# Performance work log

Hardware: AMD Instinct MI355X
Metric: run time of the kernel (lower is better)

The kernel has to match this reference:

```python
import jax, jax.numpy as jnp
import numpy as np

N, E, D, L = 20000, 320000, 3072, 64
H = D // 2  # 1536
EPS = 1e-5


def setup_inputs() -> dict:
    key = jax.random.key(0)
    ks = jax.random.split(key, 16)
    inp = {
        "x": jax.random.normal(ks[0], (N, D), dtype=jnp.float32),
        "edge_index": jax.random.randint(ks[1], (2, E), 0, N, dtype=jnp.int64),
        # GCNConv weights (x @ W + b)
        "W_gc1": jax.random.normal(ks[2], (D, H), dtype=jnp.float32) / np.sqrt(D),
        "b_gc1": jnp.zeros((H,), dtype=jnp.float32),
        "W_gc2": jax.random.normal(ks[3], (H, L), dtype=jnp.float32) / np.sqrt(H),
        "b_gc2": jnp.zeros((L,), dtype=jnp.float32),
        # LayerNorm params
        "g1": jnp.ones((H,), dtype=jnp.float32),
        "be1": jnp.zeros((H,), dtype=jnp.float32),
        "g2": jnp.ones((L,), dtype=jnp.float32),
        "be2": jnp.zeros((L,), dtype=jnp.float32),
        # Decoder Linears (PyTorch: y = x @ W.T + b; store as [in, out])
        "W_fc1": jax.random.normal(ks[4], (L, H), dtype=jnp.float32) / np.sqrt(L),
        "b_fc1": jnp.zeros((H,), dtype=jnp.float32),
        "W_fc2": jax.random.normal(ks[5], (H, D), dtype=jnp.float32) / np.sqrt(H),
        "b_fc2": jnp.zeros((D,), dtype=jnp.float32),
    }
    return inp


def _layernorm(h, g, b):
    mu = jnp.mean(h, axis=-1, keepdims=True)
    var = jnp.mean(jnp.square(h - mu), axis=-1, keepdims=True)
    return (h - mu) * jax.lax.rsqrt(var + EPS) * g + b


def _gcn_norm(edge_index, n):
    # PyG GCNConv default: add self-loops, symmetric normalization
    loop = jnp.arange(n, dtype=edge_index.dtype)
    src = jnp.concatenate([edge_index[0], loop])  # [E+N]
    dst = jnp.concatenate([edge_index[1], loop])
    deg = jax.ops.segment_sum(jnp.ones_like(dst, dtype=jnp.float32), dst, num_segments=n)
    dinv = jax.lax.rsqrt(jnp.maximum(deg, 1e-12))
    norm = dinv[src] * dinv[dst]  # [E+N]
    return src, dst, norm


def _gcn_conv(h, W, b, src, dst, norm, n):
    h = h @ W                                 # [N, out]
    m = h[src] * norm[:, None]                # gather + scale over edges
    out = jax.ops.segment_sum(m, dst, num_segments=n)  # scatter-add
    return out + b


def reference(x, edge_index, W_gc1, b_gc1, W_gc2, b_gc2, g1, be1, g2, be2,
              W_fc1, b_fc1, W_fc2, b_fc2):
    n = x.shape[0]
    src, dst, norm = _gcn_norm(edge_index, n)
    hidden = jax.nn.relu(_gcn_conv(x, W_gc1, b_gc1, src, dst, norm, n))
    hidden = _layernorm(hidden, g1, be1)
    latent = jax.nn.relu(_gcn_conv(hidden, W_gc2, b_gc2, src, dst, norm, n))
    latent = _layernorm(latent, g2, be2)
    decode = jax.nn.relu(latent @ W_fc1 + b_fc1)
    reconstructed = decode @ W_fc2 + b_fc2
    return latent, reconstructed
```

## Files before the change

### kernel.cpp

```cpp
#include <hip/hip_runtime.h>
#include <hip/hip_bf16.h>

#define NN 20000
#define EE 320000
#define DD 3072
#define HH 1536
#define LL 64

typedef unsigned short bf16_t;
typedef __attribute__((ext_vector_type(8))) __bf16 bf16x8;
typedef __attribute__((ext_vector_type(4))) float  f32x4;

__device__ __forceinline__ bf16_t f2bf(float f) {
    union { float f; unsigned u; } c; c.f = f;
    unsigned u = c.u;
    return (bf16_t)((u + 0x7fffu + ((u >> 16) & 1u)) >> 16);
}

__global__ void zero_int(int* __restrict__ p, int n) {
    int i = blockIdx.x * blockDim.x + threadIdx.x;
    if (i < n) p[i] = 0;
}

__global__ void cnt_count(const int* __restrict__ ei, int* __restrict__ cnt, int E) {
    int i = blockIdx.x * blockDim.x + threadIdx.x;
    if (i < E) atomicAdd(&cnt[ei[E + i]], 1);
}

__global__ void dinv_from_cnt(const int* __restrict__ cnt, float* __restrict__ dinv, int n) {
    int i = blockIdx.x * blockDim.x + threadIdx.x;
    if (i < n) dinv[i] = rsqrtf((float)(cnt[i] + 1));
}

__global__ __launch_bounds__(1024) void scan_rowptr(const int* __restrict__ cnt,
                                                    int* __restrict__ rowptr, int n)
{
    __shared__ int sdata[1024];
    __shared__ int scarry;
    const int tid = threadIdx.x;
    if (tid == 0) scarry = 0;
    __syncthreads();
    for (int base = 0; base < n; base += 1024) {
        int i = base + tid;
        int v = (i < n) ? cnt[i] : 0;
        int x = v;
        sdata[tid] = x;
        __syncthreads();
#pragma unroll
        for (int off = 1; off < 1024; off <<= 1) {
            int y = (tid >= off) ? sdata[tid - off] : 0;
            __syncthreads();
            x += y;
            sdata[tid] = x;
            __syncthreads();
        }
        if (i < n) rowptr[i] = scarry + x - v;
        int total = sdata[1023];
        __syncthreads();
        if (tid == 0) scarry += total;
        __syncthreads();
    }
    if (tid == 0) rowptr[n] = scarry;
}

__global__ void csr_fill(const int* __restrict__ ei, const int* __restrict__ rowptr,
                         int* __restrict__ cursor, int* __restrict__ csr_src, int E)
{
    int e = blockIdx.x * blockDim.x + threadIdx.x;
    if (e < E) {
        int d = ei[E + e];
        int pos = rowptr[d] + atomicAdd(&cursor[d], 1);
        csr_src[pos] = ei[e];
    }
}

__global__ void cvt_bf16(const float4* __restrict__ in, ushort4* __restrict__ out, long long n4) {
    for (long long i = (long long)blockIdx.x * blockDim.x + threadIdx.x;
         i < n4; i += (long long)gridDim.x * blockDim.x) {
        float4 v = in[i];
        ushort4 o;
        o.x = f2bf(v.x); o.y = f2bf(v.y); o.z = f2bf(v.z); o.w = f2bf(v.w);
        out[i] = o;
    }
}

__global__ __launch_bounds__(256) void cvt_transpose_bf16(
    const float* __restrict__ in, bf16_t* __restrict__ out, int R, int C)
{
    __shared__ float tile[32][33];
    const int bx = blockIdx.x, by = blockIdx.y;
    const int tx = threadIdx.x & 31;
    const int ty = (threadIdx.x >> 5) * 4;
#pragma unroll
    for (int j = 0; j < 4; ++j)
        tile[ty + j][tx] = in[(long long)(by * 32 + ty + j) * C + bx * 32 + tx];
    __syncthreads();
#pragma unroll
    for (int j = 0; j < 4; ++j)
        out[(long long)(bx * 32 + ty + j) * R + by * 32 + tx] = f2bf(tile[tx][ty + j]);
}

#define GLOAD_LDS16(g, l)                                                     \
    __builtin_amdgcn_global_load_lds(                                         \
        (const __attribute__((address_space(1))) unsigned int*)(g),          \
        (__attribute__((address_space(3))) unsigned int*)(l), 16, 0, 0)

#define MFMA16(a, b, c) __builtin_amdgcn_mfma_f32_16x16x32_bf16((a), (b), (c), 0, 0, 0)

#define LDA_F(CUR, MH, MF, KS)                                                \
    (*(const bf16x8*)((const char*)(&lds[(CUR)][0][(MH)][0]) +                \
        (arow + (MF) * 16) * 128 + ((KS) ? offk1 : offk0)))
#define LDB_F(CUR, NH, NF, KS)                                                \
    (*(const bf16x8*)((const char*)(&lds[(CUR)][1][(NH)][0]) +                \
        (brw + (NF) * 16) * 128 + ((KS) ? offk1 : offk0)))

#define READ_A(CUR, MH)                                                        \
    _Pragma("unroll")                                                          \
    for (int mf = 0; mf < 4; ++mf) {                                           \
        pa[mf][0] = LDA_F(CUR, MH, mf, 0);                                     \
        pa[mf][1] = LDA_F(CUR, MH, mf, 1);                                     \
    }

#define READ_B(CUR, NH)                                                        \
    _Pragma("unroll")                                                          \
    for (int nf = 0; nf < 2; ++nf) {                                           \
        pb[nf][0] = LDB_F(CUR, NH, nf, 0);                                     \
        pb[nf][1] = LDB_F(CUR, NH, nf, 1);                                     \
    }

#define PHASE_TAIL(MH, NH, STAGE_STMT, DOVM)                                   \
    do {                                                                       \
        STAGE_STMT;                                                            \
        __builtin_amdgcn_sched_barrier(0);                                     \
        __builtin_amdgcn_s_barrier();                                          \
        asm volatile("s_waitcnt lgkmcnt(0)" ::: "memory");                     \
        __builtin_amdgcn_sched_barrier(0);                                     \
        __builtin_amdgcn_s_setprio(1);                                         \
        _Pragma("unroll")                                                      \
        for (int mf = 0; mf < 4; ++mf) {                                       \
            _Pragma("unroll")                                                  \
            for (int nf = 0; nf < 2; ++nf) {                                   \
                acc[MH][NH][mf][nf] = MFMA16(pa[mf][0], pb[nf][0], acc[MH][NH][mf][nf]); \
                acc[MH][NH][mf][nf] = MFMA16(pa[mf][1], pb[nf][1], acc[MH][NH][mf][nf]); \
            }                                                                  \
        }                                                                      \
        __builtin_amdgcn_s_setprio(0);                                         \
        if (DOVM) { asm volatile("s_waitcnt vmcnt(4)" ::: "memory"); }         \
        __builtin_amdgcn_sched_barrier(0);                                     \
        __builtin_amdgcn_s_barrier();                                          \
    } while (0)

template <int HAS_BIAS, int RELU, int OUT_BF16>
__global__ __launch_bounds__(512, 2) void gemm_bf16_8ph(
    const bf16_t* __restrict__ A, const bf16_t* __restrict__ Bt,
    const float* __restrict__ bias, void* __restrict__ Cout,
    int M, int N, int K, int gx)
{
    __shared__ bf16_t lds[2][2][2][8192];

    const int nwg = gridDim.x;
    const int q = nwg >> 3, r = nwg & 7;
    const int xcd = blockIdx.x & 7, lo = blockIdx.x >> 3;
    const int wgid = (xcd < r ? xcd * (q + 1) : r * (q + 1) + (xcd - r) * q) + lo;
    const int brow = (wgid / gx) * 256;
    const int bcol = (wgid % gx) * 256;

    const int tid = threadIdx.x;
    const int w = tid >> 6, l = tid & 63;
    const int wr = w >> 2, wc = w & 3;
    const int nt = K >> 6;

    f32x4 acc[2][2][4][2] = {};

    const int srow8 = l >> 3;
    const int swz8  = (((l & 7) ^ (l >> 3)) << 3);

    auto stage_a = [&](int buf, int h, int s) {
#pragma unroll
        for (int i = 0; i < 2; ++i) {
            const int c = (w << 1) + i;
            int grow = brow + h * 128 + c * 8 + srow8;
            if (grow > M - 1) grow = M - 1;
            const bf16_t* g = A + (long long)grow * K + (s << 6) + swz8;
            GLOAD_LDS16(g, &lds[buf][0][h][c * 512]);
        }
    };
    auto stage_b = [&](int buf, int h, int s) {
#pragma unroll
        for (int i = 0; i < 2; ++i) {
            const int c = (w << 1) + i;
            const int grow = bcol + h * 128 + c * 8 + srow8;
            const bf16_t* g = Bt + (long long)grow * K + (s << 6) + swz8;
            GLOAD_LDS16(g, &lds[buf][1][h][c * 512]);
        }
    };

    const int arow  = wr * 64 + (l & 15);
    const int brw   = wc * 32 + (l & 15);
    const int xm    = (l & 7) << 4;
    const int offk0 = ((l >> 4) << 4) ^ xm;
    const int offk1 = (((l >> 4) << 4) + 64) ^ xm;

    stage_a(0, 0, 0); stage_b(0, 0, 0);
    stage_a(0, 1, 0); stage_b(0, 1, 0);
    stage_a(1, 0, 1); stage_b(1, 0, 1);
    __builtin_amdgcn_sched_barrier(0);
    asm volatile("s_waitcnt vmcnt(4)" ::: "memory");
    __builtin_amdgcn_sched_barrier(0);
    __builtin_amdgcn_s_barrier();

    int cur = 0;
    for (int t = 0; t < nt; ++t) {
        const int t1 = (t + 1 < nt) ? t + 1 : nt - 1;
        const int t2 = (t + 2 < nt) ? t + 2 : nt - 1;
        bf16x8 pa[4][2], pb[2][2];
        READ_A(cur, 0); READ_B(cur, 0);
        PHASE_TAIL(0, 0, stage_a(cur ^ 1, 1, t1), 0);
        READ_B(cur, 1);
        PHASE_TAIL(0, 1, stage_b(cur ^ 1, 1, t1), 0);
        READ_A(cur, 1);
        PHASE_TAIL(1, 1, stage_a(cur, 0, t2), 0);
        READ_B(cur, 0);
        PHASE_TAIL(1, 0, stage_b(cur, 0, t2), 1);
        cur ^= 1;
    }

#pragma unroll
    for (int mh = 0; mh < 2; ++mh) {
#pragma unroll
        for (int nh = 0; nh < 2; ++nh) {
#pragma unroll
            for (int nf = 0; nf < 2; ++nf) {
                const int col = bcol + nh * 128 + wc * 32 + nf * 16 + (l & 15);
                const float bv = HAS_BIAS ? bias[col] : 0.0f;
#pragma unroll
                for (int mf = 0; mf < 4; ++mf) {
#pragma unroll
                    for (int j = 0; j < 4; ++j) {
                        const int row = brow + mh * 128 + wr * 64 + mf * 16 + (l >> 4) * 4 + j;
                        if (row < M) {
                            float v = acc[mh][nh][mf][nf][j] + bv;
                            if (RELU) v = fmaxf(v, 0.0f);
                            if (OUT_BF16) ((bf16_t*)Cout)[(long long)row * N + col] = f2bf(v);
                            else          ((float*)Cout)[(long long)row * N + col] = v;
                        }
                    }
                }
            }
        }
    }
}

template <int HAS_BIAS, int RELU, int OUT_BF16, int BNT>
__global__ __launch_bounds__(256) void gemm_bf16_mfma(
    const bf16_t* __restrict__ A, const bf16_t* __restrict__ Bt,
    const float* __restrict__ bias, void* __restrict__ Cout,
    int M, int N, int K, int gx)
{
    constexpr int NFRAG = BNT / 32;
    constexpr int BHALF = BNT / 64;
    constexpr int WCOFF = BNT / 2;

    __shared__ bf16_t As[128 * 32];
    __shared__ bf16_t Bs[BNT * 32];

    const int nwg = gridDim.x;
    const int q = nwg >> 3, r = nwg & 7;
    const int xcd = blockIdx.x & 7, lo = blockIdx.x >> 3;
    const int wgid = (xcd < r ? xcd * (q + 1) : r * (q + 1) + (xcd - r) * q) + lo;
    const int brow = (wgid / gx) * 128;
    const int bcol = (wgid % gx) * BNT;

    const int tid = threadIdx.x;
    const int w   = tid >> 6;
    const int l   = tid & 63;
    const int wr  = w >> 1, wc = w & 1;

    f32x4 acc[4][NFRAG] = {};

    const int srow   = tid >> 2;
    const int schunk = (tid & 3) * 8;

    for (int k0 = 0; k0 < K; k0 += 32) {
#pragma unroll
        for (int half = 0; half < 2; ++half) {
            int gr = brow + half * 64 + srow;
            if (gr > M - 1) gr = M - 1;
            const bf16_t* gsrc = A + (long long)gr * K + k0 + schunk;
            GLOAD_LDS16(gsrc, &As[(half * 64 + w * 16) * 32]);
        }
#pragma unroll
        for (int half = 0; half < BHALF; ++half) {
            int rr = half * 64 + srow;
            const bf16_t* gsrc = Bt + (long long)(bcol + rr) * K + k0 + schunk;
            GLOAD_LDS16(gsrc, &Bs[(half * 64 + w * 16) * 32]);
        }
        __syncthreads();

        bf16x8 af[4], bfr[NFRAG];
#pragma unroll
        for (int m = 0; m < 4; ++m) {
            int row = wr * 64 + m * 16 + (l & 15);
            af[m] = *(const bf16x8*)&As[row * 32 + (l >> 4) * 8];
        }
#pragma unroll
        for (int n = 0; n < NFRAG; ++n) {
            int row = wc * WCOFF + n * 16 + (l & 15);
            bfr[n] = *(const bf16x8*)&Bs[row * 32 + (l >> 4) * 8];
        }
#pragma unroll
        for (int m = 0; m < 4; ++m)
#pragma unroll
            for (int n = 0; n < NFRAG; ++n)
                acc[m][n] = MFMA16(af[m], bfr[n], acc[m][n]);
        __syncthreads();
    }

#pragma unroll
    for (int m = 0; m < 4; ++m) {
#pragma unroll
        for (int n = 0; n < NFRAG; ++n) {
            int col = bcol + wc * WCOFF + n * 16 + (l & 15);
            float b = HAS_BIAS ? bias[col] : 0.0f;
#pragma unroll
            for (int j = 0; j < 4; ++j) {
                int row = brow + wr * 64 + m * 16 + (l >> 4) * 4 + j;
                if (row < M) {
                    float v = acc[m][n][j] + b;
                    if (RELU) v = fmaxf(v, 0.0f);
                    if (OUT_BF16) ((bf16_t*)Cout)[(long long)row * N + col] = f2bf(v);
                    else          ((float*)Cout)[(long long)row * N + col] = v;
                }
            }
        }
    }
}

__global__ __launch_bounds__(256) void gcn_agg_ln_h(
    const bf16_t* __restrict__ h, const float* __restrict__ dinv,
    const int* __restrict__ rowptr, const int* __restrict__ csr_src,
    const float* __restrict__ bias, const float* __restrict__ g,
    const float* __restrict__ be, bf16_t* __restrict__ out, int n)
{
    const int row  = blockIdx.x * 4 + (threadIdx.x >> 6);
    const int lane = threadIdx.x & 63;
    if (row >= n) return;
    const float dd = dinv[row];

    float acc[24];
    {
        const bf16x8* hr = (const bf16x8*)(h + (long long)row * HH);
#pragma unroll
        for (int c = 0; c < 3; ++c) {
            bf16x8 v = hr[c * 64 + lane];
#pragma unroll
            for (int j = 0; j < 8; ++j) acc[c * 8 + j] = dd * (float)v[j];
        }
    }
    const int s0 = rowptr[row], s1 = rowptr[row + 1];
    for (int k = s0; k < s1; ++k) {
        const int s = csr_src[k];
        const float w = dinv[s];
        const bf16x8* hs = (const bf16x8*)(h + (long long)s * HH);
#pragma unroll
        for (int c = 0; c < 3; ++c) {
            bf16x8 v = hs[c * 64 + lane];
#pragma unroll
            for (int j = 0; j < 8; ++j) acc[c * 8 + j] += w * (float)v[j];
        }
    }

    float lsum = 0.0f, lsq = 0.0f;
#pragma unroll
    for (int c = 0; c < 3; ++c)
#pragma unroll
        for (int j = 0; j < 8; ++j) {
            int idx = c * 512 + lane * 8 + j;
            float v = fmaxf(acc[c * 8 + j] * dd + bias[idx], 0.0f);
            acc[c * 8 + j] = v;
            lsum += v;
            lsq  += v * v;
        }
#pragma unroll
    for (int off = 32; off > 0; off >>= 1) {
        lsum += __shfl_xor(lsum, off);
        lsq  += __shfl_xor(lsq,  off);
    }
    const float mean = lsum / HH;
    const float var  = lsq / HH - mean * mean;
    const float rstd = rsqrtf(var + 1e-5f);

    bf16_t* y = out + (long long)row * HH;
#pragma unroll
    for (int c = 0; c < 3; ++c)
#pragma unroll
        for (int j = 0; j < 8; ++j) {
            int idx = c * 512 + lane * 8 + j;
            y[idx] = f2bf((acc[c * 8 + j] - mean) * rstd * g[idx] + be[idx]);
        }
}

__global__ __launch_bounds__(256) void gcn_agg_ln_l(
    const float* __restrict__ h, const float* __restrict__ dinv,
    const int* __restrict__ rowptr, const int* __restrict__ csr_src,
    const float* __restrict__ bias, const float* __restrict__ g,
    const float* __restrict__ be, float* __restrict__ out,
    bf16_t* __restrict__ outb, int n)
{
    const int row  = blockIdx.x * 4 + (threadIdx.x >> 6);
    const int lane = threadIdx.x & 63;
    if (row >= n) return;
    const float dd = dinv[row];

    float acc = dd * h[(long long)row * LL + lane];
    const int s0 = rowptr[row], s1 = rowptr[row + 1];
    for (int k = s0; k < s1; ++k) {
        const int s = csr_src[k];
        acc += dinv[s] * h[(long long)s * LL + lane];
    }
    float v = fmaxf(acc * dd + bias[lane], 0.0f);
    float lsum = v, lsq = v * v;
#pragma unroll
    for (int off = 32; off > 0; off >>= 1) {
        lsum += __shfl_xor(lsum, off);
        lsq  += __shfl_xor(lsq,  off);
    }
    const float mean = lsum / LL;
    const float var  = lsq / LL - mean * mean;
    const float rstd = rsqrtf(var + 1e-5f);
    float o = (v - mean) * rstd * g[lane] + be[lane];
    out[(long long)row * LL + lane]  = o;
    outb[(long long)row * LL + lane] = f2bf(o);
}

extern "C" void kernel_launch(void* const* d_in, const int* in_sizes, int n_in,
                              void* d_out, int out_size, void* d_ws, size_t ws_size,
                              hipStream_t stream)
{
    const float* x     = (const float*)d_in[0];
    const int*   ei    = (const int*)d_in[1];
    const float* W_gc1 = (const float*)d_in[2];
    const float* b_gc1 = (const float*)d_in[3];
    const float* W_gc2 = (const float*)d_in[4];
    const float* b_gc2 = (const float*)d_in[5];
    const float* g1    = (const float*)d_in[6];
    const float* be1   = (const float*)d_in[7];
    const float* g2    = (const float*)d_in[8];
    const float* be2   = (const float*)d_in[9];
    const float* W_fc1 = (const float*)d_in[10];
    const float* b_fc1 = (const float*)d_in[11];
    const float* W_fc2 = (const float*)d_in[12];
    const float* b_fc2 = (const float*)d_in[13];

    float* out_latent = (float*)d_out;
    float* out_recon  = (float*)d_out + (long long)NN * LL;

    bf16_t* h1b     = (bf16_t*)out_recon;
    bf16_t* hiddenb = (bf16_t*)(out_recon + (long long)NN * HH);

    float*  dinv    = (float*)d_ws;
    int*    cnt     = (int*)(dinv + NN);
    int*    cursor  = cnt + NN;
    int*    rowptr  = cursor + NN;
    int*    csr_src = rowptr + NN + 1;
    char*   pbase   = (char*)(csr_src + EE);
    pbase = (char*)(((size_t)pbase + 255) & ~(size_t)255);
    bf16_t* xb      = (bf16_t*)pbase;
    bf16_t* W1t     = xb + (long long)NN * DD;
    bf16_t* W2t     = W1t + (long long)DD * HH;
    bf16_t* Wg2t    = W2t + (long long)DD * HH;
    bf16_t* Wf1t    = Wg2t + (long long)HH * LL;
    bf16_t* latentb = Wf1t + (long long)LL * HH;
    float*  wsC     = (float*)(latentb + (long long)NN * LL);
    bf16_t* decodeb = xb;

    zero_int<<<(2 * NN + 255) / 256, 256, 0, stream>>>(cnt, 2 * NN);
    cnt_count<<<(EE + 255) / 256, 256, 0, stream>>>(ei, cnt, EE);
    dinv_from_cnt<<<(NN + 255) / 256, 256, 0, stream>>>(cnt, dinv, NN);
    scan_rowptr<<<1, 1024, 0, stream>>>(cnt, rowptr, NN);
    csr_fill<<<(EE + 255) / 256, 256, 0, stream>>>(ei, rowptr, cursor, csr_src, EE);

    cvt_bf16<<<2048, 256, 0, stream>>>((const float4*)x, (ushort4*)xb, (long long)NN * DD / 4);
    {
        dim3 ga(HH / 32, DD / 32);
        cvt_transpose_bf16<<<ga, 256, 0, stream>>>(W_gc1, W1t, DD, HH);
        dim3 gb(DD / 32, HH / 32);
        cvt_transpose_bf16<<<gb, 256, 0, stream>>>(W_fc2, W2t, HH, DD);
        dim3 gc(LL / 32, HH / 32);
        cvt_transpose_bf16<<<gc, 256, 0, stream>>>(W_gc2, Wg2t, HH, LL);
        dim3 gd(HH / 32, LL / 32);
        cvt_transpose_bf16<<<gd, 256, 0, stream>>>(W_fc1, Wf1t, LL, HH);
    }

    const int MB128 = (NN + 127) / 128;
    const int MB256 = (NN + 255) / 256;

    {
        int gx = HH / 256;
        gemm_bf16_8ph<0, 0, 1><<<gx * MB256, 512, 0, stream>>>(xb, W1t, nullptr, h1b, NN, HH, DD, gx);
    }

    gcn_agg_ln_h<<<(NN + 3) / 4, 256, 0, stream>>>(h1b, dinv, rowptr, csr_src, b_gc1, g1, be1, hiddenb, NN);

    gemm_bf16_mfma<0, 0, 0, 64><<<MB128, 256, 0, stream>>>(hiddenb, Wg2t, nullptr, wsC, NN, LL, HH, 1);

    gcn_agg_ln_l<<<(NN + 3) / 4, 256, 0, stream>>>(wsC, dinv, rowptr, csr_src, b_gc2, g2, be2, out_latent, latentb, NN);

    {
        int gx = HH / 128;
        gemm_bf16_mfma<1, 1, 1, 128><<<gx * MB128, 256, 0, stream>>>(latentb, Wf1t, b_fc1, decodeb, NN, HH, LL, gx);
    }

    {
        int gx = DD / 256;
        gemm_bf16_8ph<1, 0, 0><<<gx * MB256, 512, 0, stream>>>(decodeb, W2t, b_fc2, out_recon, NN, DD, HH, gx);
    }
}
```

Measured before the change: 804.1 us.

## Reorder GEMM main-loop phases to reuse A fragments and drop extra barriers

The bf16 GEMM main loop now holds both A half-fragments (pa0, pa1) in registers and reorders the four MFMA quadrants to 00, 10, 11, 01. This lets each quadrant reuse fragments already loaded and cuts the LDS reads per iteration. Each phase now ends with a single barrier, and the explicit lgkmcnt(0) wait and pre-MFMA barrier are gone, so LDS reads, global-to-LDS staging and MFMAs can overlap more. The cost is extra VGPR pressure under launch_bounds(512,2), and correctness now depends on compiler-inserted waits and the new buffer-reuse ordering.

```diff
diff --git a/kernel.cpp b/kernel.cpp
--- a/kernel.cpp
+++ b/kernel.cpp
@@ -114,40 +114,32 @@
     (*(const bf16x8*)((const char*)(&lds[(CUR)][1][(NH)][0]) +                \
         (brw + (NF) * 16) * 128 + ((KS) ? offk1 : offk0)))
 
-#define READ_A(CUR, MH)                                                        \
+#define READ_AQ(DST, CUR, MH)                                                  \
     _Pragma("unroll")                                                          \
     for (int mf = 0; mf < 4; ++mf) {                                           \
-        pa[mf][0] = LDA_F(CUR, MH, mf, 0);                                     \
-        pa[mf][1] = LDA_F(CUR, MH, mf, 1);                                     \
-    }
-
-#define READ_B(CUR, NH)                                                        \
+        DST[mf][0] = LDA_F(CUR, MH, mf, 0);                                    \
+        DST[mf][1] = LDA_F(CUR, MH, mf, 1);                                    \
+    }
+
+#define READ_BQ(DST, CUR, NH)                                                  \
     _Pragma("unroll")                                                          \
     for (int nf = 0; nf < 2; ++nf) {                                           \
-        pb[nf][0] = LDB_F(CUR, NH, nf, 0);                                     \
-        pb[nf][1] = LDB_F(CUR, NH, nf, 1);                                     \
-    }
-
-#define PHASE_TAIL(MH, NH, STAGE_STMT, DOVM)                                   \
+        DST[nf][0] = LDB_F(CUR, NH, nf, 0);                                    \
+        DST[nf][1] = LDB_F(CUR, NH, nf, 1);                                    \
+    }
+
+#define MFMA_Q(MH, NH, PA, PB)                                                 \
     do {                                                                       \
-        STAGE_STMT;                                                            \
-        __builtin_amdgcn_sched_barrier(0);                                     \
-        __builtin_amdgcn_s_barrier();                                          \
-        asm volatile("s_waitcnt lgkmcnt(0)" ::: "memory");                     \
-        __builtin_amdgcn_sched_barrier(0);                                     \
         __builtin_amdgcn_s_setprio(1);                                         \
         _Pragma("unroll")                                                      \
         for (int mf = 0; mf < 4; ++mf) {                                       \
             _Pragma("unroll")                                                  \
             for (int nf = 0; nf < 2; ++nf) {                                   \
-                acc[MH][NH][mf][nf] = MFMA16(pa[mf][0], pb[nf][0], acc[MH][NH][mf][nf]); \
-                acc[MH][NH][mf][nf] = MFMA16(pa[mf][1], pb[nf][1], acc[MH][NH][mf][nf]); \
+                acc[MH][NH][mf][nf] = MFMA16(PA[mf][0], PB[nf][0], acc[MH][NH][mf][nf]); \
+                acc[MH][NH][mf][nf] = MFMA16(PA[mf][1], PB[nf][1], acc[MH][NH][mf][nf]); \
             }                                                                  \
         }                                                                      \
         __builtin_amdgcn_s_setprio(0);                                         \
-        if (DOVM) { asm volatile("s_waitcnt vmcnt(4)" ::: "memory"); }         \
-        __builtin_amdgcn_sched_barrier(0);                                     \
-        __builtin_amdgcn_s_barrier();                                          \
     } while (0)
 
 template <int HAS_BIAS, int RELU, int OUT_BF16>
@@ -213,15 +205,34 @@
     for (int t = 0; t < nt; ++t) {
         const int t1 = (t + 1 < nt) ? t + 1 : nt - 1;
         const int t2 = (t + 2 < nt) ? t + 2 : nt - 1;
-        bf16x8 pa[4][2], pb[2][2];
-        READ_A(cur, 0); READ_B(cur, 0);
-        PHASE_TAIL(0, 0, stage_a(cur ^ 1, 1, t1), 0);
-        READ_B(cur, 1);
-        PHASE_TAIL(0, 1, stage_b(cur ^ 1, 1, t1), 0);
-        READ_A(cur, 1);
-        PHASE_TAIL(1, 1, stage_a(cur, 0, t2), 0);
-        READ_B(cur, 0);
-        PHASE_TAIL(1, 0, stage_b(cur, 0, t2), 1);
+        bf16x8 pa0[4][2], pa1[4][2], pb[2][2];
+
+        __builtin_amdgcn_sched_barrier(0);
+        READ_AQ(pa0, cur, 0);
+        READ_BQ(pb,  cur, 0);
+        stage_a(cur ^ 1, 1, t1);
+        MFMA_Q(0, 0, pa0, pb);
+        __builtin_amdgcn_s_barrier();
+
+        __builtin_amdgcn_sched_barrier(0);
+        READ_AQ(pa1, cur, 1);
+        stage_b(cur ^ 1, 1, t1);
+        MFMA_Q(1, 0, pa1, pb);
+        __builtin_amdgcn_s_barrier();
+
+        __builtin_amdgcn_sched_barrier(0);
+        READ_BQ(pb, cur, 1);
+        stage_a(cur, 0, t2);
+        MFMA_Q(1, 1, pa1, pb);
+        __builtin_amdgcn_s_barrier();
+
+        __builtin_amdgcn_sched_barrier(0);
+        stage_b(cur, 0, t2);
+        MFMA_Q(0, 1, pa0, pb);
+        asm volatile("s_waitcnt vmcnt(4)" ::: "memory");
+        __builtin_amdgcn_sched_barrier(0);
+        __builtin_amdgcn_s_barrier();
+
         cur ^= 1;
     }
 
```

Result: faster. 781.6 us (-2.8%).
